# Kernel tuning notes

Hardware: AMD Instinct MI355X
Metric: run time of the kernel (lower is better)

The kernel has to match this reference:

```python
import jax, jax.numpy as jnp
import numpy as np

N_HEAD = 8
HID = 256
V_DIM = HID // N_HEAD
NQ = 2048
NK = 2048
BATCH = 16
LOCALITY = 50.0  # percentile threshold; <=100 enables local masking


def setup_inputs() -> dict:
    key = jax.random.key(0)
    k1, k2, k3, k4 = jax.random.split(key, 4)
    m_dist = jax.random.uniform(k1, (N_HEAD, NQ, NK), dtype=jnp.float32)
    x = jax.random.normal(k2, (BATCH, NK, HID), dtype=jnp.float32)
    r = jax.random.normal(k3, (N_HEAD, 1, 1), dtype=jnp.float32)
    weight = jax.random.normal(k4, (N_HEAD, HID, V_DIM), dtype=jnp.float32) / jnp.sqrt(
        jnp.float32(HID)
    )
    return {"m_dist": m_dist, "x": x, "r": r, "weight": weight}


def reference(m_dist, x, r, weight):
    # distance scaling: tan(pi/4 * (1-eps) * (1 + sin(r))), per head
    scale = jnp.tan(0.25 * jnp.pi * (1.0 - 1e-07) * (1.0 + jnp.sin(r)))  # [H,1,1]
    scaled = m_dist * scale  # [H, Nq, Nk]
    # percentile-threshold local masking per (head, query) row
    thr = jnp.percentile(scaled, LOCALITY, axis=-1, keepdims=True)  # [H, Nq, 1]
    scaled = jnp.where(scaled <= thr, scaled, jnp.inf)
    att = jax.nn.softmax(-scaled, axis=-1)  # [H, Nq, Nk]
    value = jnp.einsum("bnj,hjk->bhnk", x, weight)  # [B, H, Nk, v]
    out = jnp.einsum("hjn,bhnk->bhjk", att, value)  # [B, H, Nq, v]
    out = jnp.transpose(out, (0, 2, 1, 3)).reshape(out.shape[0], out.shape[2], -1)
    return jax.nn.gelu(out)  # [B, Nq, HID]
```

## Files before the change

### kernel.cpp

```cpp
#include <hip/hip_runtime.h>
#include <hip/hip_bf16.h>

#define NH   8
#define HID  256
#define VD   32
#define NQ   2048
#define NKK  2048
#define NB   16
#define NN   512

typedef short bf16x8 __attribute__((ext_vector_type(8)));
typedef float f32x4 __attribute__((ext_vector_type(4)));

__device__ inline unsigned short f2bf(float f) {
  unsigned int u = __float_as_uint(f);
  u += 0x7FFFu + ((u >> 16) & 1u);
  return (unsigned short)(u >> 16);
}

__device__ inline void gload_lds16(const void* g, void* l) {
  __builtin_amdgcn_global_load_lds(
      (const __attribute__((address_space(1))) void*)g,
      (__attribute__((address_space(3))) void*)l, 16, 0, 0);
}

__device__ inline float gelu_f(float x) {
  float u2 = 1.5957691216057308f * (x + 0.044715f * x * x * x);
  float e = __expf(u2);
  return 0.5f * x * (1.0f + (e - 1.0f) / (e + 1.0f));
}


__global__ __launch_bounds__(256) void wt_kernel(
    const float* __restrict__ w, unsigned short* __restrict__ wT) {
  const int n = blockIdx.x;
  const int j = threadIdx.x;
  wT[(size_t)n * HID + j] = f2bf(w[(size_t)(n >> 5) * HID * VD + (size_t)j * VD + (n & 31)]);
}

__global__ __launch_bounds__(256) void value_kernel(
    const unsigned short* __restrict__ wT, const float* __restrict__ x,
    unsigned short* __restrict__ vT) {
  const int hvt = blockIdx.x & 1;
  const int kt  = blockIdx.x >> 1;
  const int b   = blockIdx.y;
  const int m0 = hvt * 128;
  const int n0 = kt * 128;
  const int t = threadIdx.x;
  const int lane = t & 63, wid = t >> 6;
  const int wr = wid >> 1, wc = wid & 1;

  __shared__ __align__(16) unsigned short As[128 * 32];
  __shared__ __align__(16) unsigned short Bs[128 * 32];

  const int rowL = t >> 2;
  const int cb = (((t & 3) ^ ((t >> 3) & 3)) * 8);
  const unsigned short* gA0 = wT + (size_t)(m0 + rowL) * HID + cb;
  const unsigned short* gA1 = gA0 + (size_t)64 * HID;
  char* lA0 = (char*)As + t * 16;
  char* lA1 = (char*)As + 4096 + t * 16;

  const int brow = t >> 1, bj = (t & 1) * 16;
  const float* gB = x + ((size_t)b * NKK + n0 + brow) * HID + bj;
  const int bc = (brow >> 1) & 3;
  const int bs0 = (2 * (t & 1)) ^ bc;
  unsigned short* lB0 = Bs + brow * 32 + bs0 * 8;
  unsigned short* lB1 = Bs + brow * 32 + (bs0 ^ 1) * 8;

  f32x4 acc[4][4];
#pragma unroll
  for (int i = 0; i < 4; ++i)
#pragma unroll
    for (int j = 0; j < 4; ++j) acc[i][j] = (f32x4){0.f, 0.f, 0.f, 0.f};

  const int fr = lane & 15;
  const int kb = (((lane >> 4) ^ ((fr >> 1) & 3)) * 16);
  const char* baseA = (const char*)As + (wr * 64 + fr) * 64 + kb;
  const char* baseB = (const char*)Bs + (wc * 64 + fr) * 64 + kb;

  f32x4 p0 = *(const f32x4*)(gB + 0);
  f32x4 p1 = *(const f32x4*)(gB + 4);
  f32x4 p2 = *(const f32x4*)(gB + 8);
  f32x4 p3 = *(const f32x4*)(gB + 12);

  for (int kk = 0; kk < HID / 32; ++kk) {
    gload_lds16(gA0, lA0);
    gload_lds16(gA1, lA1);
    gA0 += 32; gA1 += 32;

    f32x4 c0 = p0, c1 = p1, c2 = p2, c3 = p3;
    if (kk < HID / 32 - 1) {
      const float* nb = gB + (kk + 1) * 32;
      p0 = *(const f32x4*)(nb + 0);
      p1 = *(const f32x4*)(nb + 4);
      p2 = *(const f32x4*)(nb + 8);
      p3 = *(const f32x4*)(nb + 12);
    }
    uint4 pk0, pk1;
    pk0.x = (unsigned)f2bf(c0[0]) | ((unsigned)f2bf(c0[1]) << 16);
    pk0.y = (unsigned)f2bf(c0[2]) | ((unsigned)f2bf(c0[3]) << 16);
    pk0.z = (unsigned)f2bf(c1[0]) | ((unsigned)f2bf(c1[1]) << 16);
    pk0.w = (unsigned)f2bf(c1[2]) | ((unsigned)f2bf(c1[3]) << 16);
    pk1.x = (unsigned)f2bf(c2[0]) | ((unsigned)f2bf(c2[1]) << 16);
    pk1.y = (unsigned)f2bf(c2[2]) | ((unsigned)f2bf(c2[3]) << 16);
    pk1.z = (unsigned)f2bf(c3[0]) | ((unsigned)f2bf(c3[1]) << 16);
    pk1.w = (unsigned)f2bf(c3[2]) | ((unsigned)f2bf(c3[3]) << 16);
    *(uint4*)lB0 = pk0;
    *(uint4*)lB1 = pk1;

    __syncthreads();

    bf16x8 a[4], bfr[4];
#pragma unroll
    for (int i = 0; i < 4; ++i) a[i] = *(const bf16x8*)(baseA + i * 16 * 64);
#pragma unroll
    for (int j = 0; j < 4; ++j) bfr[j] = *(const bf16x8*)(baseB + j * 16 * 64);
#pragma unroll
    for (int i = 0; i < 4; ++i)
#pragma unroll
      for (int j = 0; j < 4; ++j)
        acc[i][j] = __builtin_amdgcn_mfma_f32_16x16x32_bf16(a[i], bfr[j], acc[i][j], 0, 0, 0);
    __syncthreads();
  }

  const int hvb = m0 + wr * 64 + (lane >> 4) * 4;
  const int kc0 = n0 + wc * 64 + (lane & 15);
#pragma unroll
  for (int i = 0; i < 4; ++i) {
#pragma unroll
    for (int j = 0; j < 4; ++j) {
      int kc = kc0 + j * 16;
#pragma unroll
      for (int e = 0; e < 4; ++e) {
        int hv = hvb + i * 16 + e;
        int h = hv >> 5, v = hv & 31;
        vT[((size_t)h * NN + b * VD + v) * NKK + kc] = f2bf(acc[i][j][e]);
      }
    }
  }
}

__global__ __launch_bounds__(256) void att_kernel(
    const float* __restrict__ m_dist, const float* __restrict__ r,
    unsigned short* __restrict__ att) {
  const int row = blockIdx.x;
  const int h = row >> 11;
  const int t = threadIdx.x;
  const int wid = t >> 6;
  const float* md = m_dist + (size_t)row * NKK;

  __shared__ unsigned int hist[256];
  __shared__ float coll[160];
  __shared__ unsigned int collCnt;
  __shared__ int sBA, sBB;
  __shared__ unsigned int sBelow;
  __shared__ unsigned int wtot[4];
  __shared__ float wmin[4], wsumsh[4];
  __shared__ float sVa, sVb;

  float rr = r[h];
  const float C = (float)(0.25 * 3.141592653589793 * (1.0 - 1e-7));
  float sc = tanf(C * (1.0f + sinf(rr)));

  hist[t] = 0u;
  if (t == 0) collCnt = 0u;
  __syncthreads();

  float m[8];
#pragma unroll
  for (int j = 0; j < 8; ++j) m[j] = md[t + 256 * j];

  float mn = m[0];
#pragma unroll
  for (int j = 1; j < 8; ++j) mn = fminf(mn, m[j]);
#pragma unroll
  for (int j = 0; j < 8; ++j) {
    int bin = (int)(m[j] * 256.0f);
    bin = min(max(bin, 0), 255);
    atomicAdd(&hist[bin], 1u);
  }
#pragma unroll
  for (int off = 32; off > 0; off >>= 1) mn = fminf(mn, __shfl_down(mn, off));
  if ((t & 63) == 0) wmin[wid] = mn;
  __syncthreads();

  unsigned int c = hist[t];
  unsigned int xs2 = c;
  for (int off = 1; off < 64; off <<= 1) {
    unsigned int y = __shfl_up(xs2, off);
    if ((t & 63) >= off) xs2 += y;
  }
  if ((t & 63) == 63) wtot[wid] = xs2;
  __syncthreads();
  unsigned int base = 0;
  for (int wq = 0; wq < 4; ++wq)
    if (wq < wid) base += wtot[wq];
  unsigned int cum = xs2 + base;
  if (cum >= 1024u && cum - c < 1024u) { sBA = t; sBelow = cum - c; }
  if (cum >= 1025u && cum - c < 1025u) { sBB = t; }
  __syncthreads();

  const int bA = sBA, bB = sBB;
  const unsigned int below = sBelow;
#pragma unroll
  for (int j = 0; j < 8; ++j) {
    int bin = (int)(m[j] * 256.0f);
    bin = min(max(bin, 0), 255);
    if (bin >= bA && bin <= bB) {
      unsigned int idx = atomicAdd(&collCnt, 1u);
      if (idx < 160u) coll[idx] = m[j];
    }
  }
  __syncthreads();
  const int n = (int)min(collCnt, 160u);
  const int ra = 1023 - (int)below, rb = 1024 - (int)below;
  if (t < n) {
    float v = coll[t];
    int rank = 0;
    for (int j2 = 0; j2 < n; ++j2) {
      float u = coll[j2];
      rank += (u < v || (u == v && j2 < t)) ? 1 : 0;
    }
    if (rank == ra) sVa = v;
    if (rank == rb) sVb = v;
  }
  __syncthreads();

  float mtot = fminf(fminf(wmin[0], wmin[1]), fminf(wmin[2], wmin[3]));
  float minscaled = mtot * sc;
  float ap = sVa * sc, bp = sVb * sc;
  float thr = 0.5f * ap + 0.5f * bp;

  float wv[8];
  float wsum = 0.f;
#pragma unroll
  for (int j = 0; j < 8; ++j) {
    float s = m[j] * sc;
    float e = (s <= thr) ? __expf(minscaled - s) : 0.f;
    wv[j] = e;
    wsum += e;
  }
#pragma unroll
  for (int off = 32; off > 0; off >>= 1) wsum += __shfl_down(wsum, off);
  if ((t & 63) == 0) wsumsh[wid] = wsum;
  __syncthreads();
  float denom = wsumsh[0] + wsumsh[1] + wsumsh[2] + wsumsh[3];
  float inv = 1.0f / denom;

  unsigned short* ao = att + (size_t)row * NKK;
#pragma unroll
  for (int j = 0; j < 8; ++j) ao[t + 256 * j] = f2bf(wv[j] * inv);
}

__global__ __launch_bounds__(256) void gemm_kernel(
    const unsigned short* __restrict__ att, const unsigned short* __restrict__ vT,
    float* __restrict__ out) {
  const int bid = blockIdx.x;
  const int h = bid & 7;
  const int tile = bid >> 3;
  const int qt = tile >> 2, nt = tile & 3;
  const int q0 = qt * 128, n0 = nt * 128;
  const int t = threadIdx.x;
  const int lane = t & 63, wid = t >> 6;
  const int wr = wid >> 1, wc = wid & 1;

  __shared__ __align__(16) unsigned short As[4][128 * 32];
  __shared__ __align__(16) unsigned short Bs[4][128 * 32];

  const int rowL = t >> 2;
  const int cb = (((t & 3) ^ ((t >> 3) & 3)) * 8);

  const unsigned short* gA = att + ((size_t)h * NQ + q0 + rowL) * NKK + cb;
  const unsigned short* gB = vT + ((size_t)h * NN + n0 + rowL) * NKK + cb;
  const int ldsOff = t * 16;

#define STAGE(BI, KT) do {                                                  \
    const unsigned short* a_ = gA + (KT) * 32;                              \
    const unsigned short* b_ = gB + (KT) * 32;                              \
    char* lA_ = (char*)As[(BI)] + ldsOff;                                   \
    char* lB_ = (char*)Bs[(BI)] + ldsOff;                                   \
    gload_lds16(a_, lA_);                                                   \
    gload_lds16(a_ + (size_t)64 * NKK, lA_ + 4096);                         \
    gload_lds16(b_, lB_);                                                   \
    gload_lds16(b_ + (size_t)64 * NKK, lB_ + 4096);                         \
  } while (0)

  f32x4 acc[4][4];
#pragma unroll
  for (int i = 0; i < 4; ++i)
#pragma unroll
    for (int j = 0; j < 4; ++j) acc[i][j] = (f32x4){0.f, 0.f, 0.f, 0.f};

  const int fr = lane & 15;
  const int kb = (((lane >> 4) ^ ((fr >> 1) & 3)) * 16);
  const int fragOff = (wr * 64 + fr) * 64 + kb;
  const int fragOffB = (wc * 64 + fr) * 64 + kb;

  STAGE(0, 0);
  STAGE(1, 1);
  STAGE(2, 2);
  asm volatile("s_waitcnt vmcnt(8)\n\ts_barrier" ::: "memory");

  for (int kt = 0; kt < 64; kt += 4) {
#pragma unroll
    for (int u = 0; u < 4; ++u) {
      const char* bA = (const char*)As[u] + fragOff;
      const char* bB = (const char*)Bs[u] + fragOffB;
      bf16x8 a[4], b[4];
#pragma unroll
      for (int i = 0; i < 4; ++i) a[i] = *(const bf16x8*)(bA + i * 1024);
#pragma unroll
      for (int j = 0; j < 4; ++j) b[j] = *(const bf16x8*)(bB + j * 1024);
      STAGE((u + 3) & 3, (kt + u + 3) & 63);
#pragma unroll
      for (int i = 0; i < 4; ++i)
#pragma unroll
        for (int j = 0; j < 4; ++j)
          acc[i][j] = __builtin_amdgcn_mfma_f32_16x16x32_bf16(a[i], b[j], acc[i][j], 0, 0, 0);
      asm volatile("s_waitcnt vmcnt(8)\n\ts_barrier" ::: "memory");
    }
  }
  asm volatile("s_waitcnt vmcnt(0)" ::: "memory");
#undef STAGE

  const int orow = q0 + wr * 64 + (lane >> 4) * 4;
  const int ocol0 = n0 + wc * 64 + (lane & 15);
#pragma unroll
  for (int i = 0; i < 4; ++i) {
#pragma unroll
    for (int j = 0; j < 4; ++j) {
      int ncol = ocol0 + j * 16;
      int bb = ncol >> 5, vv = ncol & 31;
      float* op = out + ((size_t)bb * NQ + orow + i * 16) * HID + h * VD + vv;
#pragma unroll
      for (int e = 0; e < 4; ++e) op[(size_t)e * HID] = gelu_f(acc[i][j][e]);
    }
  }
}

extern "C" void kernel_launch(void* const* d_in, const int* in_sizes, int n_in,
                              void* d_out, int out_size, void* d_ws, size_t ws_size,
                              hipStream_t stream) {
  const float* m_dist = (const float*)d_in[0];
  const float* x      = (const float*)d_in[1];
  const float* r      = (const float*)d_in[2];
  const float* weight = (const float*)d_in[3];
  float* out = (float*)d_out;

  unsigned short* att = (unsigned short*)d_ws;
  unsigned short* vT  = (unsigned short*)((char*)d_ws + (size_t)NH * NQ * NKK * 2);
  unsigned short* wT  = (unsigned short*)((char*)d_ws + (size_t)NH * NQ * NKK * 2 +
                                          (size_t)NH * NN * NKK * 2);

  wt_kernel<<<dim3(256), dim3(256), 0, stream>>>(weight, wT);
  value_kernel<<<dim3(32, NB), dim3(256), 0, stream>>>(wT, x, vT);
  att_kernel<<<dim3(NH * NQ), dim3(256), 0, stream>>>(m_dist, r, att);
  gemm_kernel<<<dim3(NH * 64), dim3(256), 0, stream>>>(att, vT, out);
}
```

Measured before the change: 112.6 us.

## Fuse weight transpose, value GEMM and attention softmax into one launch

Removes the separate weight-transpose kernel by having value blocks read fp32 weights directly and convert them to bf16 into LDS. Merges the value GEMM and the per-row attention kernel into one grid with block-index dispatch, so the two independent stages run concurrently and two launches disappear. Also raises wave priority around the MFMA block in the main GEMM. The value blocks now read weights with strided scalar loads, and the shared LDS footprint may change occupancy of the attention blocks.

```diff
diff --git a/kernel.cpp b/kernel.cpp
--- a/kernel.cpp
+++ b/kernel.cpp
@@ -31,225 +31,227 @@
 }
 
 
-__global__ __launch_bounds__(256) void wt_kernel(
-    const float* __restrict__ w, unsigned short* __restrict__ wT) {
-  const int n = blockIdx.x;
-  const int j = threadIdx.x;
-  wT[(size_t)n * HID + j] = f2bf(w[(size_t)(n >> 5) * HID * VD + (size_t)j * VD + (n & 31)]);
-}
-
-__global__ __launch_bounds__(256) void value_kernel(
-    const unsigned short* __restrict__ wT, const float* __restrict__ x,
-    unsigned short* __restrict__ vT) {
-  const int hvt = blockIdx.x & 1;
-  const int kt  = blockIdx.x >> 1;
-  const int b   = blockIdx.y;
-  const int m0 = hvt * 128;
-  const int n0 = kt * 128;
+__global__ __launch_bounds__(256) void fused_va_kernel(
+    const float* __restrict__ x, const float* __restrict__ w,
+    const float* __restrict__ m_dist, const float* __restrict__ r,
+    unsigned short* __restrict__ vT, unsigned short* __restrict__ att) {
+  __shared__ __align__(16) char smem[16384];
   const int t = threadIdx.x;
-  const int lane = t & 63, wid = t >> 6;
-  const int wr = wid >> 1, wc = wid & 1;
-
-  __shared__ __align__(16) unsigned short As[128 * 32];
-  __shared__ __align__(16) unsigned short Bs[128 * 32];
-
-  const int rowL = t >> 2;
-  const int cb = (((t & 3) ^ ((t >> 3) & 3)) * 8);
-  const unsigned short* gA0 = wT + (size_t)(m0 + rowL) * HID + cb;
-  const unsigned short* gA1 = gA0 + (size_t)64 * HID;
-  char* lA0 = (char*)As + t * 16;
-  char* lA1 = (char*)As + 4096 + t * 16;
-
-  const int brow = t >> 1, bj = (t & 1) * 16;
-  const float* gB = x + ((size_t)b * NKK + n0 + brow) * HID + bj;
-  const int bc = (brow >> 1) & 3;
-  const int bs0 = (2 * (t & 1)) ^ bc;
-  unsigned short* lB0 = Bs + brow * 32 + bs0 * 8;
-  unsigned short* lB1 = Bs + brow * 32 + (bs0 ^ 1) * 8;
-
-  f32x4 acc[4][4];
-#pragma unroll
-  for (int i = 0; i < 4; ++i)
-#pragma unroll
-    for (int j = 0; j < 4; ++j) acc[i][j] = (f32x4){0.f, 0.f, 0.f, 0.f};
-
-  const int fr = lane & 15;
-  const int kb = (((lane >> 4) ^ ((fr >> 1) & 3)) * 16);
-  const char* baseA = (const char*)As + (wr * 64 + fr) * 64 + kb;
-  const char* baseB = (const char*)Bs + (wc * 64 + fr) * 64 + kb;
-
-  f32x4 p0 = *(const f32x4*)(gB + 0);
-  f32x4 p1 = *(const f32x4*)(gB + 4);
-  f32x4 p2 = *(const f32x4*)(gB + 8);
-  f32x4 p3 = *(const f32x4*)(gB + 12);
-
-  for (int kk = 0; kk < HID / 32; ++kk) {
-    gload_lds16(gA0, lA0);
-    gload_lds16(gA1, lA1);
-    gA0 += 32; gA1 += 32;
-
-    f32x4 c0 = p0, c1 = p1, c2 = p2, c3 = p3;
-    if (kk < HID / 32 - 1) {
-      const float* nb = gB + (kk + 1) * 32;
-      p0 = *(const f32x4*)(nb + 0);
-      p1 = *(const f32x4*)(nb + 4);
-      p2 = *(const f32x4*)(nb + 8);
-      p3 = *(const f32x4*)(nb + 12);
-    }
-    uint4 pk0, pk1;
-    pk0.x = (unsigned)f2bf(c0[0]) | ((unsigned)f2bf(c0[1]) << 16);
-    pk0.y = (unsigned)f2bf(c0[2]) | ((unsigned)f2bf(c0[3]) << 16);
-    pk0.z = (unsigned)f2bf(c1[0]) | ((unsigned)f2bf(c1[1]) << 16);
-    pk0.w = (unsigned)f2bf(c1[2]) | ((unsigned)f2bf(c1[3]) << 16);
-    pk1.x = (unsigned)f2bf(c2[0]) | ((unsigned)f2bf(c2[1]) << 16);
-    pk1.y = (unsigned)f2bf(c2[2]) | ((unsigned)f2bf(c2[3]) << 16);
-    pk1.z = (unsigned)f2bf(c3[0]) | ((unsigned)f2bf(c3[1]) << 16);
-    pk1.w = (unsigned)f2bf(c3[2]) | ((unsigned)f2bf(c3[3]) << 16);
-    *(uint4*)lB0 = pk0;
-    *(uint4*)lB1 = pk1;
-
-    __syncthreads();
-
-    bf16x8 a[4], bfr[4];
-#pragma unroll
-    for (int i = 0; i < 4; ++i) a[i] = *(const bf16x8*)(baseA + i * 16 * 64);
-#pragma unroll
-    for (int j = 0; j < 4; ++j) bfr[j] = *(const bf16x8*)(baseB + j * 16 * 64);
+
+  if (blockIdx.x < 512) {
+    const int vb  = blockIdx.x;
+    const int hvt = vb & 1;
+    const int kt  = (vb >> 1) & 15;
+    const int b   = vb >> 5;
+    const int m0 = hvt * 128;
+    const int n0 = kt * 128;
+    const int lane = t & 63, wid = t >> 6;
+    const int wr = wid >> 1, wc = wid & 1;
+
+    unsigned short* As = (unsigned short*)smem;
+    unsigned short* Bs = (unsigned short*)(smem + 8192);
+
+    const int arow = t >> 1;
+    const int ahalf = t & 1;
+    const int hh = (m0 + arow) >> 5, avv = (m0 + arow) & 31;
+    const float* wbase = w + ((size_t)hh * HID + ahalf * 16) * VD + avv;
+    const int ac = (arow >> 1) & 3;
+    unsigned short* wA0 = (unsigned short*)((char*)As + arow * 64 + (((2 * ahalf) ^ ac) * 16));
+    unsigned short* wA1 = (unsigned short*)((char*)As + arow * 64 + (((2 * ahalf + 1) ^ ac) * 16));
+
+    const int brow = t >> 1, bj = (t & 1) * 16;
+    const float* gB = x + ((size_t)b * NKK + n0 + brow) * HID + bj;
+    const int bc = (brow >> 1) & 3;
+    const int bs0 = (2 * (t & 1)) ^ bc;
+    unsigned short* lB0 = Bs + brow * 32 + bs0 * 8;
+    unsigned short* lB1 = Bs + brow * 32 + ((bs0 ^ 1)) * 8;
+
+    f32x4 acc[4][4];
 #pragma unroll
     for (int i = 0; i < 4; ++i)
 #pragma unroll
-      for (int j = 0; j < 4; ++j)
-        acc[i][j] = __builtin_amdgcn_mfma_f32_16x16x32_bf16(a[i], bfr[j], acc[i][j], 0, 0, 0);
-    __syncthreads();
+      for (int j = 0; j < 4; ++j) acc[i][j] = (f32x4){0.f, 0.f, 0.f, 0.f};
+
+    const int fr = lane & 15;
+    const int kb = (((lane >> 4) ^ ((fr >> 1) & 3)) * 16);
+    const char* baseA = (const char*)As + (wr * 64 + fr) * 64 + kb;
+    const char* baseB = (const char*)Bs + (wc * 64 + fr) * 64 + kb;
+
+    f32x4 p0 = *(const f32x4*)(gB + 0);
+    f32x4 p1 = *(const f32x4*)(gB + 4);
+    f32x4 p2 = *(const f32x4*)(gB + 8);
+    f32x4 p3 = *(const f32x4*)(gB + 12);
+
+    for (int kk = 0; kk < HID / 32; ++kk) {
+      float av[16];
+#pragma unroll
+      for (int e = 0; e < 16; ++e) av[e] = wbase[((size_t)kk * 32 + e) * VD];
+
+      f32x4 c0 = p0, c1 = p1, c2 = p2, c3 = p3;
+      if (kk < HID / 32 - 1) {
+        const float* nb = gB + (kk + 1) * 32;
+        p0 = *(const f32x4*)(nb + 0);
+        p1 = *(const f32x4*)(nb + 4);
+        p2 = *(const f32x4*)(nb + 8);
+        p3 = *(const f32x4*)(nb + 12);
+      }
+      uint4 qa0, qa1;
+      qa0.x = (unsigned)f2bf(av[0]) | ((unsigned)f2bf(av[1]) << 16);
+      qa0.y = (unsigned)f2bf(av[2]) | ((unsigned)f2bf(av[3]) << 16);
+      qa0.z = (unsigned)f2bf(av[4]) | ((unsigned)f2bf(av[5]) << 16);
+      qa0.w = (unsigned)f2bf(av[6]) | ((unsigned)f2bf(av[7]) << 16);
+      qa1.x = (unsigned)f2bf(av[8]) | ((unsigned)f2bf(av[9]) << 16);
+      qa1.y = (unsigned)f2bf(av[10]) | ((unsigned)f2bf(av[11]) << 16);
+      qa1.z = (unsigned)f2bf(av[12]) | ((unsigned)f2bf(av[13]) << 16);
+      qa1.w = (unsigned)f2bf(av[14]) | ((unsigned)f2bf(av[15]) << 16);
+      *(uint4*)wA0 = qa0;
+      *(uint4*)wA1 = qa1;
+
+      uint4 pk0, pk1;
+      pk0.x = (unsigned)f2bf(c0[0]) | ((unsigned)f2bf(c0[1]) << 16);
+      pk0.y = (unsigned)f2bf(c0[2]) | ((unsigned)f2bf(c0[3]) << 16);
+      pk0.z = (unsigned)f2bf(c1[0]) | ((unsigned)f2bf(c1[1]) << 16);
+      pk0.w = (unsigned)f2bf(c1[2]) | ((unsigned)f2bf(c1[3]) << 16);
+      pk1.x = (unsigned)f2bf(c2[0]) | ((unsigned)f2bf(c2[1]) << 16);
+      pk1.y = (unsigned)f2bf(c2[2]) | ((unsigned)f2bf(c2[3]) << 16);
+      pk1.z = (unsigned)f2bf(c3[0]) | ((unsigned)f2bf(c3[1]) << 16);
+      pk1.w = (unsigned)f2bf(c3[2]) | ((unsigned)f2bf(c3[3]) << 16);
+      *(uint4*)lB0 = pk0;
+      *(uint4*)lB1 = pk1;
+
+      __syncthreads();
+
+      bf16x8 a[4], bfr[4];
+#pragma unroll
+      for (int i = 0; i < 4; ++i) a[i] = *(const bf16x8*)(baseA + i * 16 * 64);
+#pragma unroll
+      for (int j = 0; j < 4; ++j) bfr[j] = *(const bf16x8*)(baseB + j * 16 * 64);
+#pragma unroll
+      for (int i = 0; i < 4; ++i)
+#pragma unroll
+        for (int j = 0; j < 4; ++j)
+          acc[i][j] = __builtin_amdgcn_mfma_f32_16x16x32_bf16(a[i], bfr[j], acc[i][j], 0, 0, 0);
+      __syncthreads();
+    }
+
+    const int hvb = m0 + wr * 64 + (lane >> 4) * 4;
+    const int kc0 = n0 + wc * 64 + (lane & 15);
+#pragma unroll
+    for (int i = 0; i < 4; ++i) {
+#pragma unroll
+      for (int j = 0; j < 4; ++j) {
+        int kc = kc0 + j * 16;
+#pragma unroll
+        for (int e = 0; e < 4; ++e) {
+          int hv = hvb + i * 16 + e;
+          int h = hv >> 5, v = hv & 31;
+          vT[((size_t)h * NN + b * VD + v) * NKK + kc] = f2bf(acc[i][j][e]);
+        }
+      }
+    }
+  } else {
+    const int row = blockIdx.x - 512;
+    const int h = row >> 11;
+    const int wid = t >> 6;
+    const float* md = m_dist + (size_t)row * NKK;
+
+    unsigned int* hist = (unsigned int*)smem;
+    float* coll = (float*)(smem + 1024);
+    unsigned int* su = (unsigned int*)(smem + 1664);
+    float* sf = (float*)(smem + 1696);
+
+    float rr = r[h];
+    const float C = (float)(0.25 * 3.141592653589793 * (1.0 - 1e-7));
+    float sc = tanf(C * (1.0f + sinf(rr)));
+
+    hist[t] = 0u;
+    if (t == 0) su[0] = 0u;
+    __syncthreads();
+
+    float m[8];
+#pragma unroll
+    for (int j = 0; j < 8; ++j) m[j] = md[t + 256 * j];
+
+    float mn = m[0];
+#pragma unroll
+    for (int j = 1; j < 8; ++j) mn = fminf(mn, m[j]);
+#pragma unroll
+    for (int j = 0; j < 8; ++j) {
+      int bin = (int)(m[j] * 256.0f);
+      bin = min(max(bin, 0), 255);
+      atomicAdd(&hist[bin], 1u);
+    }
+#pragma unroll
+    for (int off = 32; off > 0; off >>= 1) mn = fminf(mn, __shfl_down(mn, off));
+    if ((t & 63) == 0) sf[wid] = mn;
+    __syncthreads();
+
+    unsigned int c = hist[t];
+    unsigned int xs2 = c;
+    for (int off = 1; off < 64; off <<= 1) {
+      unsigned int y = __shfl_up(xs2, off);
+      if ((t & 63) >= off) xs2 += y;
+    }
+    if ((t & 63) == 63) su[4 + wid] = xs2;
+    __syncthreads();
+    unsigned int base = 0;
+    for (int wq = 0; wq < 4; ++wq)
+      if (wq < wid) base += su[4 + wq];
+    unsigned int cum = xs2 + base;
+    if (cum >= 1024u && cum - c < 1024u) { su[1] = (unsigned)t; su[3] = cum - c; }
+    if (cum >= 1025u && cum - c < 1025u) { su[2] = (unsigned)t; }
+    __syncthreads();
+
+    const int bA = (int)su[1], bB = (int)su[2];
+    const unsigned int below = su[3];
+#pragma unroll
+    for (int j = 0; j < 8; ++j) {
+      int bin = (int)(m[j] * 256.0f);
+      bin = min(max(bin, 0), 255);
+      if (bin >= bA && bin <= bB) {
+        unsigned int idx = atomicAdd(&su[0], 1u);
+        if (idx < 160u) coll[idx] = m[j];
+      }
+    }
+    __syncthreads();
+    const int n = (int)min(su[0], 160u);
+    const int ra = 1023 - (int)below, rb = 1024 - (int)below;
+    if (t < n) {
+      float v = coll[t];
+      int rank = 0;
+      for (int j2 = 0; j2 < n; ++j2) {
+        float u = coll[j2];
+        rank += (u < v || (u == v && j2 < t)) ? 1 : 0;
+      }
+      if (rank == ra) sf[8] = v;
+      if (rank == rb) sf[9] = v;
+    }
+    __syncthreads();
+
+    float mtot = fminf(fminf(sf[0], sf[1]), fminf(sf[2], sf[3]));
+    float minscaled = mtot * sc;
+    float thr = 0.5f * (sf[8] * sc) + 0.5f * (sf[9] * sc);
+
+    float wv[8];
+    float wsum = 0.f;
+#pragma unroll
+    for (int j = 0; j < 8; ++j) {
+      float s = m[j] * sc;
+      float e = (s <= thr) ? __expf(minscaled - s) : 0.f;
+      wv[j] = e;
+      wsum += e;
+    }
+#pragma unroll
+    for (int off = 32; off > 0; off >>= 1) wsum += __shfl_down(wsum, off);
+    if ((t & 63) == 0) sf[4 + wid] = wsum;
+    __syncthreads();
+    float denom = sf[4] + sf[5] + sf[6] + sf[7];
+    float inv = 1.0f / denom;
+
+    unsigned short* ao = att + (size_t)row * NKK;
+#pragma unroll
+    for (int j = 0; j < 8; ++j) ao[t + 256 * j] = f2bf(wv[j] * inv);
   }
-
-  const int hvb = m0 + wr * 64 + (lane >> 4) * 4;
-  const int kc0 = n0 + wc * 64 + (lane & 15);
-#pragma unroll
-  for (int i = 0; i < 4; ++i) {
-#pragma unroll
-    for (int j = 0; j < 4; ++j) {
-      int kc = kc0 + j * 16;
-#pragma unroll
-      for (int e = 0; e < 4; ++e) {
-        int hv = hvb + i * 16 + e;
-        int h = hv >> 5, v = hv & 31;
-        vT[((size_t)h * NN + b * VD + v) * NKK + kc] = f2bf(acc[i][j][e]);
-      }
-    }
-  }
-}
-
-__global__ __launch_bounds__(256) void att_kernel(
-    const float* __restrict__ m_dist, const float* __restrict__ r,
-    unsigned short* __restrict__ att) {
-  const int row = blockIdx.x;
-  const int h = row >> 11;
-  const int t = threadIdx.x;
-  const int wid = t >> 6;
-  const float* md = m_dist + (size_t)row * NKK;
-
-  __shared__ unsigned int hist[256];
-  __shared__ float coll[160];
-  __shared__ unsigned int collCnt;
-  __shared__ int sBA, sBB;
-  __shared__ unsigned int sBelow;
-  __shared__ unsigned int wtot[4];
-  __shared__ float wmin[4], wsumsh[4];
-  __shared__ float sVa, sVb;
-
-  float rr = r[h];
-  const float C = (float)(0.25 * 3.141592653589793 * (1.0 - 1e-7));
-  float sc = tanf(C * (1.0f + sinf(rr)));
-
-  hist[t] = 0u;
-  if (t == 0) collCnt = 0u;
-  __syncthreads();
-
-  float m[8];
-#pragma unroll
-  for (int j = 0; j < 8; ++j) m[j] = md[t + 256 * j];
-
-  float mn = m[0];
-#pragma unroll
-  for (int j = 1; j < 8; ++j) mn = fminf(mn, m[j]);
-#pragma unroll
-  for (int j = 0; j < 8; ++j) {
-    int bin = (int)(m[j] * 256.0f);
-    bin = min(max(bin, 0), 255);
-    atomicAdd(&hist[bin], 1u);
-  }
-#pragma unroll
-  for (int off = 32; off > 0; off >>= 1) mn = fminf(mn, __shfl_down(mn, off));
-  if ((t & 63) == 0) wmin[wid] = mn;
-  __syncthreads();
-
-  unsigned int c = hist[t];
-  unsigned int xs2 = c;
-  for (int off = 1; off < 64; off <<= 1) {
-    unsigned int y = __shfl_up(xs2, off);
-    if ((t & 63) >= off) xs2 += y;
-  }
-  if ((t & 63) == 63) wtot[wid] = xs2;
-  __syncthreads();
-  unsigned int base = 0;
-  for (int wq = 0; wq < 4; ++wq)
-    if (wq < wid) base += wtot[wq];
-  unsigned int cum = xs2 + base;
-  if (cum >= 1024u && cum - c < 1024u) { sBA = t; sBelow = cum - c; }
-  if (cum >= 1025u && cum - c < 1025u) { sBB = t; }
-  __syncthreads();
-
-  const int bA = sBA, bB = sBB;
-  const unsigned int below = sBelow;
-#pragma unroll
-  for (int j = 0; j < 8; ++j) {
-    int bin = (int)(m[j] * 256.0f);
-    bin = min(max(bin, 0), 255);
-    if (bin >= bA && bin <= bB) {
-      unsigned int idx = atomicAdd(&collCnt, 1u);
-      if (idx < 160u) coll[idx] = m[j];
-    }
-  }
-  __syncthreads();
-  const int n = (int)min(collCnt, 160u);
-  const int ra = 1023 - (int)below, rb = 1024 - (int)below;
-  if (t < n) {
-    float v = coll[t];
-    int rank = 0;
-    for (int j2 = 0; j2 < n; ++j2) {
-      float u = coll[j2];
-      rank += (u < v || (u == v && j2 < t)) ? 1 : 0;
-    }
-    if (rank == ra) sVa = v;
-    if (rank == rb) sVb = v;
-  }
-  __syncthreads();
-
-  float mtot = fminf(fminf(wmin[0], wmin[1]), fminf(wmin[2], wmin[3]));
-  float minscaled = mtot * sc;
-  float ap = sVa * sc, bp = sVb * sc;
-  float thr = 0.5f * ap + 0.5f * bp;
-
-  float wv[8];
-  float wsum = 0.f;
-#pragma unroll
-  for (int j = 0; j < 8; ++j) {
-    float s = m[j] * sc;
-    float e = (s <= thr) ? __expf(minscaled - s) : 0.f;
-    wv[j] = e;
-    wsum += e;
-  }
-#pragma unroll
-  for (int off = 32; off > 0; off >>= 1) wsum += __shfl_down(wsum, off);
-  if ((t & 63) == 0) wsumsh[wid] = wsum;
-  __syncthreads();
-  float denom = wsumsh[0] + wsumsh[1] + wsumsh[2] + wsumsh[3];
-  float inv = 1.0f / denom;
-
-  unsigned short* ao = att + (size_t)row * NKK;
-#pragma unroll
-  for (int j = 0; j < 8; ++j) ao[t + 256 * j] = f2bf(wv[j] * inv);
 }
 
 __global__ __launch_bounds__(256) void gemm_kernel(
@@ -312,11 +314,13 @@
 #pragma unroll
       for (int j = 0; j < 4; ++j) b[j] = *(const bf16x8*)(bB + j * 1024);
       STAGE((u + 3) & 3, (kt + u + 3) & 63);
+      __builtin_amdgcn_s_setprio(1);
 #pragma unroll
       for (int i = 0; i < 4; ++i)
 #pragma unroll
         for (int j = 0; j < 4; ++j)
           acc[i][j] = __builtin_amdgcn_mfma_f32_16x16x32_bf16(a[i], b[j], acc[i][j], 0, 0, 0);
+      __builtin_amdgcn_s_setprio(0);
       asm volatile("s_waitcnt vmcnt(8)\n\ts_barrier" ::: "memory");
     }
   }
@@ -349,11 +353,7 @@
 
   unsigned short* att = (unsigned short*)d_ws;
   unsigned short* vT  = (unsigned short*)((char*)d_ws + (size_t)NH * NQ * NKK * 2);
-  unsigned short* wT  = (unsigned short*)((char*)d_ws + (size_t)NH * NQ * NKK * 2 +
-                                          (size_t)NH * NN * NKK * 2);
-
-  wt_kernel<<<dim3(256), dim3(256), 0, stream>>>(weight, wT);
-  value_kernel<<<dim3(32, NB), dim3(256), 0, stream>>>(wT, x, vT);
-  att_kernel<<<dim3(NH * NQ), dim3(256), 0, stream>>>(m_dist, r, att);
+
+  fused_va_kernel<<<dim3(512 + NH * NQ), dim3(256), 0, stream>>>(x, weight, m_dist, r, vT, att);
   gemm_kernel<<<dim3(NH * 64), dim3(256), 0, stream>>>(att, vT, out);
 }
```

Result: slower. 144.4 us (+28.3%).

## Process one attention row per wavefront and prioritize MFMA issue in GEMM

Applied to the files above, without the earlier changes.

The attention-row kernel now assigns one row per 64-lane wavefront instead of one per 256-thread block. It replaces block-wide barriers and cross-wave shared reductions with wave-level shuffles, ballots and per-wave LDS histograms, and uses vectorized float4 loads and packed bf16 stores. The GEMM inner loop raises wave priority around the MFMA block with s_setprio. The goal is to remove synchronization overhead and narrow memory transactions in the memory-bound softmax/percentile pass, at the cost of more registers per lane and a serial rank loop over up to three collision slots per lane.

```diff
diff --git a/kernel.cpp b/kernel.cpp
--- a/kernel.cpp
+++ b/kernel.cpp
@@ -143,113 +143,124 @@
 __global__ __launch_bounds__(256) void att_kernel(
     const float* __restrict__ m_dist, const float* __restrict__ r,
     unsigned short* __restrict__ att) {
-  const int row = blockIdx.x;
+  const int w = threadIdx.x >> 6;
+  const int lane = threadIdx.x & 63;
+  const int row = (blockIdx.x << 2) | w;
   const int h = row >> 11;
-  const int t = threadIdx.x;
-  const int wid = t >> 6;
+
+  __shared__ unsigned int histS[4][256];
+  __shared__ float collS[4][160];
+  __shared__ unsigned int cntS[4];
+  __shared__ float vabS[4][2];
+
+  unsigned int* hist = histS[w];
+  float* coll = collS[w];
+
+  const float C = (float)(0.25 * 3.141592653589793 * (1.0 - 1e-7));
+  float sc = tanf(C * (1.0f + sinf(r[h])));
+
+  *(uint4*)&hist[lane * 4] = (uint4){0u, 0u, 0u, 0u};
+  if (lane == 0) cntS[w] = 0u;
+
   const float* md = m_dist + (size_t)row * NKK;
-
-  __shared__ unsigned int hist[256];
-  __shared__ float coll[160];
-  __shared__ unsigned int collCnt;
-  __shared__ int sBA, sBB;
-  __shared__ unsigned int sBelow;
-  __shared__ unsigned int wtot[4];
-  __shared__ float wmin[4], wsumsh[4];
-  __shared__ float sVa, sVb;
-
-  float rr = r[h];
-  const float C = (float)(0.25 * 3.141592653589793 * (1.0 - 1e-7));
-  float sc = tanf(C * (1.0f + sinf(rr)));
-
-  hist[t] = 0u;
-  if (t == 0) collCnt = 0u;
-  __syncthreads();
-
-  float m[8];
-#pragma unroll
-  for (int j = 0; j < 8; ++j) m[j] = md[t + 256 * j];
-
-  float mn = m[0];
-#pragma unroll
-  for (int j = 1; j < 8; ++j) mn = fminf(mn, m[j]);
-#pragma unroll
-  for (int j = 0; j < 8; ++j) {
-    int bin = (int)(m[j] * 256.0f);
-    bin = min(max(bin, 0), 255);
-    atomicAdd(&hist[bin], 1u);
-  }
-#pragma unroll
-  for (int off = 32; off > 0; off >>= 1) mn = fminf(mn, __shfl_down(mn, off));
-  if ((t & 63) == 0) wmin[wid] = mn;
-  __syncthreads();
-
-  unsigned int c = hist[t];
-  unsigned int xs2 = c;
+  f32x4 m4[8];
+#pragma unroll
+  for (int k = 0; k < 8; ++k) m4[k] = *(const f32x4*)(md + 4 * lane + 256 * k);
+
+  float mn = 1e30f;
+#pragma unroll
+  for (int k = 0; k < 8; ++k)
+#pragma unroll
+    for (int e = 0; e < 4; ++e) {
+      float v = m4[k][e];
+      mn = fminf(mn, v);
+      int bin = min(max((int)(v * 256.0f), 0), 255);
+      atomicAdd(&hist[bin], 1u);
+    }
+#pragma unroll
+  for (int off = 32; off; off >>= 1) mn = fminf(mn, __shfl_xor(mn, off));
+
+  asm volatile("s_waitcnt lgkmcnt(0)" ::: "memory");
+  uint4 hc = *(const uint4*)&hist[lane * 4];
+  unsigned c0 = hc.x, c1 = hc.x + hc.y, c2 = c1 + hc.z, c3 = c2 + hc.w;
+  unsigned g = c3;
+  unsigned incl = g;
+#pragma unroll
   for (int off = 1; off < 64; off <<= 1) {
-    unsigned int y = __shfl_up(xs2, off);
-    if ((t & 63) >= off) xs2 += y;
-  }
-  if ((t & 63) == 63) wtot[wid] = xs2;
-  __syncthreads();
-  unsigned int base = 0;
-  for (int wq = 0; wq < 4; ++wq)
-    if (wq < wid) base += wtot[wq];
-  unsigned int cum = xs2 + base;
-  if (cum >= 1024u && cum - c < 1024u) { sBA = t; sBelow = cum - c; }
-  if (cum >= 1025u && cum - c < 1025u) { sBB = t; }
-  __syncthreads();
-
-  const int bA = sBA, bB = sBB;
-  const unsigned int below = sBelow;
-#pragma unroll
-  for (int j = 0; j < 8; ++j) {
-    int bin = (int)(m[j] * 256.0f);
-    bin = min(max(bin, 0), 255);
-    if (bin >= bA && bin <= bB) {
-      unsigned int idx = atomicAdd(&collCnt, 1u);
-      if (idx < 160u) coll[idx] = m[j];
-    }
-  }
-  __syncthreads();
-  const int n = (int)min(collCnt, 160u);
+    unsigned y = __shfl_up(incl, off);
+    if (lane >= off) incl += y;
+  }
+  unsigned excl = incl - g;
+
+  unsigned long long ba1 = __ballot(incl >= 1024u);
+  int glA = __ffsll((unsigned long long)ba1) - 1;
+  unsigned eA = __shfl(excl, glA);
+  unsigned a0 = __shfl(excl + c0, glA), a1 = __shfl(excl + c1, glA), a2 = __shfl(excl + c2, glA);
+  int bA; unsigned below;
+  if (a0 >= 1024u)      { bA = glA * 4 + 0; below = eA; }
+  else if (a1 >= 1024u) { bA = glA * 4 + 1; below = a0; }
+  else if (a2 >= 1024u) { bA = glA * 4 + 2; below = a1; }
+  else                  { bA = glA * 4 + 3; below = a2; }
+  unsigned long long ba2 = __ballot(incl >= 1025u);
+  int glB = __ffsll((unsigned long long)ba2) - 1;
+  unsigned e0 = __shfl(excl + c0, glB), e1 = __shfl(excl + c1, glB), e2 = __shfl(excl + c2, glB);
+  int bB = (e0 >= 1025u) ? glB * 4 : (e1 >= 1025u) ? glB * 4 + 1
+                                   : (e2 >= 1025u) ? glB * 4 + 2 : glB * 4 + 3;
+
+#pragma unroll
+  for (int k = 0; k < 8; ++k)
+#pragma unroll
+    for (int e = 0; e < 4; ++e) {
+      float v = m4[k][e];
+      int bin = min(max((int)(v * 256.0f), 0), 255);
+      if (bin >= bA && bin <= bB) {
+        unsigned idx = atomicAdd(&cntS[w], 1u);
+        if (idx < 160u) coll[idx] = v;
+      }
+    }
+  asm volatile("s_waitcnt lgkmcnt(0)" ::: "memory");
+  const int n = (int)min(cntS[w], 160u);
   const int ra = 1023 - (int)below, rb = 1024 - (int)below;
-  if (t < n) {
-    float v = coll[t];
-    int rank = 0;
-    for (int j2 = 0; j2 < n; ++j2) {
-      float u = coll[j2];
-      rank += (u < v || (u == v && j2 < t)) ? 1 : 0;
-    }
-    if (rank == ra) sVa = v;
-    if (rank == rb) sVb = v;
-  }
-  __syncthreads();
-
-  float mtot = fminf(fminf(wmin[0], wmin[1]), fminf(wmin[2], wmin[3]));
-  float minscaled = mtot * sc;
-  float ap = sVa * sc, bp = sVb * sc;
-  float thr = 0.5f * ap + 0.5f * bp;
-
-  float wv[8];
+#pragma unroll
+  for (int e2 = 0; e2 < 3; ++e2) {
+    int idx = lane + (e2 << 6);
+    if (idx < n) {
+      float v = coll[idx];
+      int rank = 0;
+      for (int j2 = 0; j2 < n; ++j2) {
+        float u = coll[j2];
+        rank += (u < v || (u == v && j2 < idx)) ? 1 : 0;
+      }
+      if (rank == ra) vabS[w][0] = v;
+      if (rank == rb) vabS[w][1] = v;
+    }
+  }
+  asm volatile("s_waitcnt lgkmcnt(0)" ::: "memory");
+  float thr = 0.5f * (vabS[w][0] * sc) + 0.5f * (vabS[w][1] * sc);
+  float minscaled = mn * sc;
+
   float wsum = 0.f;
 #pragma unroll
-  for (int j = 0; j < 8; ++j) {
-    float s = m[j] * sc;
-    float e = (s <= thr) ? __expf(minscaled - s) : 0.f;
-    wv[j] = e;
-    wsum += e;
-  }
-#pragma unroll
-  for (int off = 32; off > 0; off >>= 1) wsum += __shfl_down(wsum, off);
-  if ((t & 63) == 0) wsumsh[wid] = wsum;
-  __syncthreads();
-  float denom = wsumsh[0] + wsumsh[1] + wsumsh[2] + wsumsh[3];
-  float inv = 1.0f / denom;
+  for (int k = 0; k < 8; ++k)
+#pragma unroll
+    for (int e = 0; e < 4; ++e) {
+      float s = m4[k][e] * sc;
+      float ev = (s <= thr) ? __expf(minscaled - s) : 0.f;
+      m4[k][e] = ev;
+      wsum += ev;
+    }
+#pragma unroll
+  for (int off = 32; off; off >>= 1) wsum += __shfl_xor(wsum, off);
+  float inv = 1.0f / wsum;
 
   unsigned short* ao = att + (size_t)row * NKK;
 #pragma unroll
-  for (int j = 0; j < 8; ++j) ao[t + 256 * j] = f2bf(wv[j] * inv);
+  for (int k = 0; k < 8; ++k) {
+    uint2 pk;
+    pk.x = (unsigned)f2bf(m4[k][0] * inv) | ((unsigned)f2bf(m4[k][1] * inv) << 16);
+    pk.y = (unsigned)f2bf(m4[k][2] * inv) | ((unsigned)f2bf(m4[k][3] * inv) << 16);
+    *(uint2*)(ao + 4 * lane + 256 * k) = pk;
+  }
 }
 
 __global__ __launch_bounds__(256) void gemm_kernel(
@@ -312,11 +323,13 @@
 #pragma unroll
       for (int j = 0; j < 4; ++j) b[j] = *(const bf16x8*)(bB + j * 1024);
       STAGE((u + 3) & 3, (kt + u + 3) & 63);
+      __builtin_amdgcn_s_setprio(1);
 #pragma unroll
       for (int i = 0; i < 4; ++i)
 #pragma unroll
         for (int j = 0; j < 4; ++j)
           acc[i][j] = __builtin_amdgcn_mfma_f32_16x16x32_bf16(a[i], b[j], acc[i][j], 0, 0, 0);
+      __builtin_amdgcn_s_setprio(0);
       asm volatile("s_waitcnt vmcnt(8)\n\ts_barrier" ::: "memory");
     }
   }
@@ -354,6 +367,6 @@
 
   wt_kernel<<<dim3(256), dim3(256), 0, stream>>>(weight, wT);
   value_kernel<<<dim3(32, NB), dim3(256), 0, stream>>>(wT, x, vT);
-  att_kernel<<<dim3(NH * NQ), dim3(256), 0, stream>>>(m_dist, r, att);
+  att_kernel<<<dim3(NH * NQ / 4), dim3(256), 0, stream>>>(m_dist, r, att);
   gemm_kernel<<<dim3(NH * 64), dim3(256), 0, stream>>>(att, vT, out);
 }
```

Measured after the change: 103.7 us. -7.9%, faster.
